# Kernel optimization log

Hardware: AMD Instinct MI355X
Metric: run time of the kernel (lower is better)

The kernel has to match this reference:

```python
import jax, jax.numpy as jnp
import numpy as np

B, C, IMG, PS, S, D, H, HD, L, OUT = 512, 3, 36, 6, 36, 768, 12, 64, 4, 256

def _pos_embedding(seq_len, dim):
    # NOTE: cos at even indices, sin at odd (as in the torch source)
    position = np.arange(seq_len, dtype=np.float32)[:, None]
    div = np.exp(np.arange(0, dim, 2, dtype=np.float32) * -(np.log(10000.0) / dim))
    emb = np.zeros((seq_len, dim), dtype=np.float32)
    emb[:, 0::2] = np.cos(position * div)
    emb[:, 1::2] = np.sin(position * div)
    return jnp.asarray(emb)

def setup_inputs():
    ks = jax.random.split(jax.random.key(0), 10)
    sc = lambda f: 1.0 / np.sqrt(f)
    return {
        'batch': jax.random.normal(ks[0], (B, C, IMG, IMG), jnp.float32),
        'W_patch': jax.random.normal(ks[1], (D, PS * PS), jnp.float32) * sc(PS * PS),
        'b_patch': jnp.zeros((D,), jnp.float32),
        'pos': _pos_embedding(S, D),
        'ln1_g': jnp.ones((L, D), jnp.float32),
        'ln1_b': jnp.zeros((L, D), jnp.float32),
        'Wq': jax.random.normal(ks[2], (L, H, HD, HD), jnp.float32) * sc(HD),
        'bq': jnp.zeros((L, H, HD), jnp.float32),
        'Wk': jax.random.normal(ks[3], (L, H, HD, HD), jnp.float32) * sc(HD),
        'bk': jnp.zeros((L, H, HD), jnp.float32),
        'Wv': jax.random.normal(ks[4], (L, H, HD, HD), jnp.float32) * sc(HD),
        'bv': jnp.zeros((L, H, HD), jnp.float32),
        'ln2_g': jnp.ones((L, D), jnp.float32),
        'ln2_b': jnp.zeros((L, D), jnp.float32),
        'W1': jax.random.normal(ks[5], (L, 2 * D, D), jnp.float32) * sc(D),
        'b1': jnp.zeros((L, 2 * D), jnp.float32),
        'W2': jax.random.normal(ks[6], (L, D, 2 * D), jnp.float32) * sc(2 * D),
        'b2': jnp.zeros((L, D), jnp.float32),
        'W_out': jax.random.normal(ks[7], (OUT, D), jnp.float32) * sc(D),
        'b_out': jnp.zeros((OUT,), jnp.float32),
    }

def _layernorm(x, g, b):
    m = jnp.mean(x, axis=-1, keepdims=True)
    v = jnp.mean((x - m) ** 2, axis=-1, keepdims=True)
    return (x - m) / jnp.sqrt(v + 1e-5) * g + b

def _forward(batch, W_patch, b_patch, pos, ln1_g, ln1_b, Wq, bq, Wk, bk, Wv, bv,
             ln2_g, ln2_b, W1, b1, W2, b2, W_out, b_out):
    b_, c_ = batch.shape[0], batch.shape[1]
    # patchify: (B,C,36,36) -> (B,C,36 patches,36 pixels), matching torch unfold+reshape
    p = batch.reshape(b_, c_, IMG // PS, PS, IMG // PS, PS)
    p = p.transpose(0, 1, 2, 4, 3, 5).reshape(b_, c_, S, PS * PS)
    z = p @ W_patch.T + b_patch + pos  # pos broadcasts over (B,C)
    scale = 1.0 / np.sqrt(HD)
    for l in range(L):
        # pre-LN then batched per-head attention (collapses the python loops)
        h = _layernorm(z, ln1_g[l], ln1_b[l]).reshape(b_, c_, S, H, HD)
        q = jnp.einsum('bcshd,hed->bcshe', h, Wq[l]) + bq[l]
        k = jnp.einsum('bcshd,hed->bcshe', h, Wk[l]) + bk[l]
        v = jnp.einsum('bcshd,hed->bcshe', h, Wv[l]) + bv[l]
        attn = jax.nn.softmax(jnp.einsum('bcshe,bcthe->bchst', q, k) * scale, axis=-1)
        o = jnp.einsum('bchst,bcthe->bcshe', attn, v).reshape(b_, c_, S, D)
        z = z + o
        z = _layernorm(z, ln2_g[l], ln2_b[l])
        z = z + (jax.nn.relu(z @ W1[l].T + b1[l]) @ W2[l].T + b2[l])
    return z @ W_out.T + b_out

def reference(batch, W_patch, b_patch, pos, ln1_g, ln1_b, Wq, bq, Wk, bk, Wv, bv,
              ln2_g, ln2_b, W1, b1, W2, b2, W_out, b_out):
    return _forward(batch, W_patch, b_patch, pos, ln1_g, ln1_b, Wq, bq, Wk, bk, Wv, bv,
                    ln2_g, ln2_b, W1, b1, W2, b2, W_out, b_out)
```

## Files before the change

### kernel.cpp

```cpp
#include <hip/hip_runtime.h>
#include <hip/hip_bf16.h>
#include <cstdint>
#include <cstddef>

typedef __bf16 bf16;
typedef bf16 bf16x8 __attribute__((ext_vector_type(8)));
typedef bf16 bf16x4 __attribute__((ext_vector_type(4)));
typedef float f32x4 __attribute__((ext_vector_type(4)));
typedef unsigned int u32;

#define GLD_LDS16(gptr, lptr)                                                        \
  __builtin_amdgcn_global_load_lds((const __attribute__((address_space(1))) u32*)(gptr), \
                                   (__attribute__((address_space(3))) u32*)(lptr), 16, 0, 0)

static constexpr int S = 36, D = 768, H = 12, HD = 64, DFF = 1536;
static constexpr int BC = 1536;
static constexpr int M = BC * S;
static constexpr int OUTD = 256;

__global__ __launch_bounds__(256) void f2b_kernel(const float* __restrict__ in,
                                                  bf16* __restrict__ out, int n4) {
  int i = blockIdx.x * 256 + threadIdx.x;
  if (i < n4) {
    float4 f = ((const float4*)in)[i];
    bf16x4 o = {(bf16)f.x, (bf16)f.y, (bf16)f.z, (bf16)f.w};
    ((bf16x4*)out)[i] = o;
  }
}

__global__ __launch_bounds__(64) void qk_prep(const float* __restrict__ Wq,
                                              const float* __restrict__ Wk,
                                              const float* __restrict__ bq,
                                              bf16* __restrict__ wb,
                                              float* __restrict__ vkout) {
  int lh = blockIdx.x;
  int e = threadIdx.x;
  __shared__ float Wqs[64][64];
  __shared__ float Wks[64][64];
  const float* wqp = Wq + (size_t)lh * 4096;
  const float* wkp = Wk + (size_t)lh * 4096;
  for (int i = e; i < 4096; i += 64) {
    Wqs[i >> 6][i & 63] = wqp[i];
    Wks[i >> 6][i & 63] = wkp[i];
  }
  __syncthreads();
  float ks[64];
#pragma unroll
  for (int f = 0; f < 64; ++f) ks[f] = Wks[f][e];
  for (int d0 = 0; d0 < 64; d0 += 4) {
    float a0 = 0.f, a1 = 0.f, a2 = 0.f, a3 = 0.f;
#pragma unroll
    for (int f = 0; f < 64; ++f) {
      float4 wq4 = *(const float4*)&Wqs[f][d0];
      a0 += wq4.x * ks[f]; a1 += wq4.y * ks[f];
      a2 += wq4.z * ks[f]; a3 += wq4.w * ks[f];
    }
    bf16x4 o = {(bf16)a0, (bf16)a1, (bf16)a2, (bf16)a3};
    *(bf16x4*)&wb[(size_t)lh * 4096 + e * 64 + d0] = o;
  }
  const float* bqp = bq + lh * 64;
  float acc = 0.f;
#pragma unroll
  for (int f = 0; f < 64; ++f) acc += ks[f] * bqp[f];
  vkout[lh * 64 + e] = acc;
}

__global__ __launch_bounds__(256) void patch_embed(const float* __restrict__ batch,
                                                   const float* __restrict__ Wp,
                                                   const float* __restrict__ bp,
                                                   const float* __restrict__ pos,
                                                   float* __restrict__ z) {
  int bc = blockIdx.x, tid = threadIdx.x;
  __shared__ float p[36][40];
  for (int i = tid; i < 1296; i += 256) {
    float f = batch[(size_t)bc * 1296 + i];
    int row = i / 36, col = i - row * 36;
    p[(row / 6) * 6 + col / 6][(row % 6) * 6 + (col % 6)] = f;
  }
  __syncthreads();
  for (int c0 = 0; c0 < 768; c0 += 256) {
    int d = c0 + tid;
    float wr[36];
    const float4* wp4 = (const float4*)(Wp + (size_t)d * 36);
#pragma unroll
    for (int q = 0; q < 9; ++q) {
      float4 f = wp4[q];
      wr[q * 4] = f.x; wr[q * 4 + 1] = f.y; wr[q * 4 + 2] = f.z; wr[q * 4 + 3] = f.w;
    }
    float gb = bp[d];
    for (int s = 0; s < 36; ++s) {
      float acc = 0.f;
#pragma unroll
      for (int k = 0; k < 36; ++k) acc += p[s][k] * wr[k];
      z[((size_t)bc * 36 + s) * 768 + d] = acc + gb + pos[s * 768 + d];
    }
  }
}

__global__ __launch_bounds__(256) void ln_stats(const float* __restrict__ zin,
                                                float* __restrict__ stats) {
  int row = blockIdx.x * 4 + (threadIdx.x >> 6);
  int lane = threadIdx.x & 63;
  const float* zr = zin + (size_t)row * D;
  float x[12];
#pragma unroll
  for (int i = 0; i < 12; ++i) x[i] = zr[i * 64 + lane];
  float s = 0.f;
#pragma unroll
  for (int i = 0; i < 12; ++i) s += x[i];
#pragma unroll
  for (int off = 32; off >= 1; off >>= 1) s += __shfl_xor(s, off, 64);
  float m = s * (1.f / 768.f);
  float v = 0.f;
#pragma unroll
  for (int i = 0; i < 12; ++i) { float dd = x[i] - m; v += dd * dd; }
#pragma unroll
  for (int off = 32; off >= 1; off >>= 1) v += __shfl_xor(v, off, 64);
  v *= (1.f / 768.f);
  if (lane == 0) {
    stats[(size_t)row * 2] = m;
    stats[(size_t)row * 2 + 1] = rsqrtf(v + 1e-5f);
  }
}

__global__ __launch_bounds__(256) void ln_inplace(float* __restrict__ z,
                                                  const float* __restrict__ g,
                                                  const float* __restrict__ bt) {
  int row = blockIdx.x * 4 + (threadIdx.x >> 6);
  int lane = threadIdx.x & 63;
  float* zr = z + (size_t)row * D;
  float x[12];
#pragma unroll
  for (int i = 0; i < 12; ++i) x[i] = zr[i * 64 + lane];
  float s = 0.f;
#pragma unroll
  for (int i = 0; i < 12; ++i) s += x[i];
#pragma unroll
  for (int off = 32; off >= 1; off >>= 1) s += __shfl_xor(s, off, 64);
  float m = s * (1.f / 768.f);
  float v = 0.f;
#pragma unroll
  for (int i = 0; i < 12; ++i) { float dd = x[i] - m; v += dd * dd; }
#pragma unroll
  for (int off = 32; off >= 1; off >>= 1) v += __shfl_xor(v, off, 64);
  v *= (1.f / 768.f);
  float rstd = rsqrtf(v + 1e-5f);
#pragma unroll
  for (int i = 0; i < 12; ++i) {
    int d = i * 64 + lane;
    zr[d] = (x[i] - m) * rstd * g[d] + bt[d];
  }
}

__global__ __launch_bounds__(64) void attn_kernel(const float* __restrict__ zg,
                                                  const float* __restrict__ stats,
                                                  const float* __restrict__ g1,
                                                  const float* __restrict__ b1_,
                                                  const bf16* __restrict__ Wqk,
                                                  const bf16* __restrict__ Wv,
                                                  const float* __restrict__ vk,
                                                  const float* __restrict__ bv,
                                                  float* __restrict__ z) {
  int head = blockIdx.x;
  int bc = blockIdx.y;
  __shared__ __align__(16) bf16 gb[48 * 72];
  __shared__ __align__(16) bf16 vt[64 * 72];
  int lane = threadIdx.x;
  int lr = lane & 15, quad = lane >> 4;

#pragma unroll
  for (int t0 = 0; t0 < 16; ++t0) vt[lane * 72 + 48 + t0] = (bf16)0.f;

  const float* zsrc = zg + ((size_t)bc * S) * D + head * HD;
  const float* st = stats + (size_t)bc * S * 2;

  float gv[2][8], bvv[2][8];
#pragma unroll
  for (int kt = 0; kt < 2; ++kt) {
    int c0 = head * HD + kt * 32 + quad * 8;
    float4 ga = *(const float4*)(g1 + c0);
    float4 gb2 = *(const float4*)(g1 + c0 + 4);
    float4 ba = *(const float4*)(b1_ + c0);
    float4 bb2 = *(const float4*)(b1_ + c0 + 4);
    gv[kt][0] = ga.x; gv[kt][1] = ga.y; gv[kt][2] = ga.z; gv[kt][3] = ga.w;
    gv[kt][4] = gb2.x; gv[kt][5] = gb2.y; gv[kt][6] = gb2.z; gv[kt][7] = gb2.w;
    bvv[kt][0] = ba.x; bvv[kt][1] = ba.y; bvv[kt][2] = ba.z; bvv[kt][3] = ba.w;
    bvv[kt][4] = bb2.x; bvv[kt][5] = bb2.y; bvv[kt][6] = bb2.z; bvv[kt][7] = bb2.w;
  }

  bf16x8 hfrag[3][2];
#pragma unroll
  for (int mt = 0; mt < 3; ++mt) {
    int srow = mt * 16 + lr;
    if (srow < 36) {
      float mm = st[srow * 2], rr = st[srow * 2 + 1];
#pragma unroll
      for (int kt = 0; kt < 2; ++kt) {
        int c0 = kt * 32 + quad * 8;
        float4 f0 = *(const float4*)(zsrc + (size_t)srow * D + c0);
        float4 f1 = *(const float4*)(zsrc + (size_t)srow * D + c0 + 4);
        float hv[8] = {f0.x, f0.y, f0.z, f0.w, f1.x, f1.y, f1.z, f1.w};
        bf16x8 o;
#pragma unroll
        for (int j = 0; j < 8; ++j) o[j] = (bf16)((hv[j] - mm) * rr * gv[kt][j] + bvv[kt][j]);
        hfrag[mt][kt] = o;
      }
    } else {
#pragma unroll
      for (int kt = 0; kt < 2; ++kt) {
        bf16x8 o;
#pragma unroll
        for (int j = 0; j < 8; ++j) o[j] = (bf16)0.f;
        hfrag[mt][kt] = o;
      }
    }
  }

  float vkv[2][8];
#pragma unroll
  for (int kt = 0; kt < 2; ++kt) {
    int c0 = head * 64 + kt * 32 + quad * 8;
    float4 va = *(const float4*)(vk + c0);
    float4 vb2 = *(const float4*)(vk + c0 + 4);
    vkv[kt][0] = va.x; vkv[kt][1] = va.y; vkv[kt][2] = va.z; vkv[kt][3] = va.w;
    vkv[kt][4] = vb2.x; vkv[kt][5] = vb2.y; vkv[kt][6] = vb2.z; vkv[kt][7] = vb2.w;
  }
  float tv[3];
#pragma unroll
  for (int mt = 0; mt < 3; ++mt) {
    float sp = 0.f;
#pragma unroll
    for (int kt = 0; kt < 2; ++kt)
#pragma unroll
      for (int j = 0; j < 8; ++j) sp += (float)hfrag[mt][kt][j] * vkv[kt][j];
    sp += __shfl_xor(sp, 16, 64);
    sp += __shfl_xor(sp, 32, 64);
    tv[mt] = sp;
  }

  const bf16* Wm[2] = {Wqk + (size_t)head * 4096, Wv + (size_t)head * 4096};
  const float* bvp = bv + head * 64;
  for (int p = 0; p < 2; ++p) {
    bf16x8 bfr[4][2];
#pragma unroll
    for (int nt = 0; nt < 4; ++nt)
#pragma unroll
      for (int kt = 0; kt < 2; ++kt)
        bfr[nt][kt] = *(const bf16x8*)(Wm[p] + (nt * 16 + lr) * 64 + kt * 32 + quad * 8);
#pragma unroll
    for (int mt = 0; mt < 3; ++mt) {
      f32x4 acc[4] = {};
#pragma unroll
      for (int kt = 0; kt < 2; ++kt)
#pragma unroll
        for (int nt = 0; nt < 4; ++nt)
          acc[nt] = __builtin_amdgcn_mfma_f32_16x16x32_bf16(hfrag[mt][kt], bfr[nt][kt], acc[nt], 0, 0, 0);
#pragma unroll
      for (int nt = 0; nt < 4; ++nt) {
        float bb = (p == 1) ? bvp[nt * 16 + lr] : 0.f;
#pragma unroll
        for (int r = 0; r < 4; ++r) {
          int s2 = mt * 16 + quad * 4 + r;
          int e = nt * 16 + lr;
          float val = acc[nt][r] + bb;
          if (p == 0) gb[s2 * 72 + e] = (bf16)val;
          else vt[e * 72 + s2] = (bf16)val;
        }
      }
    }
  }
  __syncthreads();

  f32x4 sc[3][3];
#pragma unroll
  for (int mt = 0; mt < 3; ++mt)
#pragma unroll
    for (int nt = 0; nt < 3; ++nt) {
      f32x4 a = {};
#pragma unroll
      for (int kt = 0; kt < 2; ++kt) {
        bf16x8 af = *(const bf16x8*)&gb[(mt * 16 + lr) * 72 + kt * 32 + quad * 8];
        a = __builtin_amdgcn_mfma_f32_16x16x32_bf16(af, hfrag[nt][kt], a, 0, 0, 0);
      }
      int t = nt * 16 + lr;
#pragma unroll
      for (int r = 0; r < 4; ++r) {
        float v = (a[r] + tv[nt]) * 0.125f;
        if (t >= 36) v = -1e30f;
        sc[mt][nt][r] = v;
      }
    }
  __syncthreads();

#pragma unroll
  for (int mt = 0; mt < 3; ++mt) {
    float mx[4], sum[4];
#pragma unroll
    for (int r = 0; r < 4; ++r)
      mx[r] = fmaxf(fmaxf(sc[mt][0][r], sc[mt][1][r]), sc[mt][2][r]);
#pragma unroll
    for (int r = 0; r < 4; ++r)
#pragma unroll
      for (int off = 8; off >= 1; off >>= 1) mx[r] = fmaxf(mx[r], __shfl_xor(mx[r], off, 64));
#pragma unroll
    for (int r = 0; r < 4; ++r) sum[r] = 0.f;
#pragma unroll
    for (int nt = 0; nt < 3; ++nt)
#pragma unroll
      for (int r = 0; r < 4; ++r) {
        float e = __expf(sc[mt][nt][r] - mx[r]);
        sc[mt][nt][r] = e;
        sum[r] += e;
      }
#pragma unroll
    for (int r = 0; r < 4; ++r)
#pragma unroll
      for (int off = 8; off >= 1; off >>= 1) sum[r] += __shfl_xor(sum[r], off, 64);
#pragma unroll
    for (int nt = 0; nt < 4; ++nt)
#pragma unroll
      for (int r = 0; r < 4; ++r) {
        int s2 = mt * 16 + quad * 4 + r;
        int t = nt * 16 + lr;
        float pv = (nt < 3) ? sc[mt][nt][r] / sum[r] : 0.f;
        gb[s2 * 72 + t] = (bf16)pv;
      }
  }
  __syncthreads();

#pragma unroll
  for (int mt = 0; mt < 3; ++mt) {
    f32x4 o[4] = {};
#pragma unroll
    for (int kt = 0; kt < 2; ++kt) {
      bf16x8 a = *(const bf16x8*)&gb[(mt * 16 + lr) * 72 + kt * 32 + quad * 8];
#pragma unroll
      for (int nt = 0; nt < 4; ++nt) {
        bf16x8 b = *(const bf16x8*)&vt[(nt * 16 + lr) * 72 + kt * 32 + quad * 8];
        o[nt] = __builtin_amdgcn_mfma_f32_16x16x32_bf16(a, b, o[nt], 0, 0, 0);
      }
    }
#pragma unroll
    for (int nt = 0; nt < 4; ++nt)
#pragma unroll
      for (int r = 0; r < 4; ++r) {
        int s2 = mt * 16 + quad * 4 + r;
        if (s2 < 36) {
          int e = nt * 16 + lr;
          size_t idx = ((size_t)bc * S + s2) * D + head * HD + e;
          z[idx] += o[nt][r];
        }
      }
  }
}

template <int N, int K, int MODE, int AF32>
__global__ __launch_bounds__(256) void gemm_bt(const void* __restrict__ A,
                                               const bf16* __restrict__ Bw,
                                               const float* __restrict__ bias,
                                               const float* __restrict__ res,
                                               void* __restrict__ outp) {
  constexpr int BK = 64;
  __shared__ __align__(16) bf16 As[128 * BK];
  __shared__ __align__(16) bf16 Bs[128 * BK];
  int tid = threadIdx.x;
  int bn = blockIdx.x, bm = blockIdx.y;
  const bf16* Abf = (const bf16*)A + (size_t)bm * 128 * K;
  const float* Af = (const float*)A + (size_t)bm * 128 * K;
  const bf16* Bb = Bw + (size_t)bn * 128 * K;
  int lane = tid & 63, wave = tid >> 6;
  int wm = (wave >> 1) * 64, wn = (wave & 1) * 64;
  int lr = lane & 15, quad = lane >> 4;
  f32x4 acc[4][4] = {};
  for (int k0 = 0; k0 < K; k0 += BK) {
    if (AF32) {
#pragma unroll
      for (int r = 0; r < 8; ++r) {
        int c = r * 256 + tid;
        int row = c >> 4, col4 = (c & 15) * 4;
        float4 f = *(const float4*)(Af + (size_t)row * K + k0 + col4);
        bf16x4 o = {(bf16)f.x, (bf16)f.y, (bf16)f.z, (bf16)f.w};
        *(bf16x4*)&As[row * BK + col4] = o;
      }
    } else {
#pragma unroll
      for (int r = 0; r < 4; ++r) {
        int c = r * 256 + tid;
        int row = c >> 3, col = (c & 7) * 8;
        GLD_LDS16(Abf + (size_t)row * K + k0 + col, &As[c * 8]);
      }
    }
#pragma unroll
    for (int r = 0; r < 4; ++r) {
      int c = r * 256 + tid;
      int row = c >> 3, col = (c & 7) * 8;
      GLD_LDS16(Bb + (size_t)row * K + k0 + col, &Bs[c * 8]);
    }
    __syncthreads();
#pragma unroll
    for (int kt = 0; kt < 2; ++kt) {
      bf16x8 af[4], bfr[4];
#pragma unroll
      for (int mt = 0; mt < 4; ++mt) af[mt] = *(const bf16x8*)&As[(wm + mt * 16 + lr) * BK + kt * 32 + quad * 8];
#pragma unroll
      for (int nt = 0; nt < 4; ++nt) bfr[nt] = *(const bf16x8*)&Bs[(wn + nt * 16 + lr) * BK + kt * 32 + quad * 8];
#pragma unroll
      for (int mt = 0; mt < 4; ++mt)
#pragma unroll
        for (int nt = 0; nt < 4; ++nt)
          acc[mt][nt] = __builtin_amdgcn_mfma_f32_16x16x32_bf16(af[mt], bfr[nt], acc[mt][nt], 0, 0, 0);
    }
    __syncthreads();
  }
  int row0 = bm * 128 + wm + quad * 4;
  int col0 = bn * 128 + wn + lr;
#pragma unroll
  for (int mt = 0; mt < 4; ++mt)
#pragma unroll
    for (int nt = 0; nt < 4; ++nt) {
      int col = col0 + nt * 16;
      float bv = bias[col];
#pragma unroll
      for (int r = 0; r < 4; ++r) {
        size_t idx = (size_t)(row0 + mt * 16 + r) * N + col;
        float v = acc[mt][nt][r] + bv;
        if (MODE == 0) ((bf16*)outp)[idx] = (bf16)fmaxf(v, 0.f);
        else if (MODE == 1) ((float*)outp)[idx] = v + res[idx];
        else ((float*)outp)[idx] = v;
      }
    }
}

extern "C" void kernel_launch(void* const* d_in, const int* in_sizes, int n_in,
                              void* d_out, int out_size, void* d_ws, size_t ws_size,
                              hipStream_t stream) {
  const float* batch   = (const float*)d_in[0];
  const float* W_patch = (const float*)d_in[1];
  const float* b_patch = (const float*)d_in[2];
  const float* pos     = (const float*)d_in[3];
  const float* ln1_g   = (const float*)d_in[4];
  const float* ln1_b   = (const float*)d_in[5];
  const float* Wq      = (const float*)d_in[6];
  const float* bq      = (const float*)d_in[7];
  const float* Wk      = (const float*)d_in[8];
  const float* bk      = (const float*)d_in[9];
  const float* Wv      = (const float*)d_in[10];
  const float* bv      = (const float*)d_in[11];
  const float* ln2_g   = (const float*)d_in[12];
  const float* ln2_b   = (const float*)d_in[13];
  const float* W1      = (const float*)d_in[14];
  const float* b1      = (const float*)d_in[15];
  const float* W2      = (const float*)d_in[16];
  const float* b2      = (const float*)d_in[17];
  const float* W_out   = (const float*)d_in[18];
  const float* b_out   = (const float*)d_in[19];
  float* out = (float*)d_out;
  (void)bk;

  char* ws = (char*)d_ws;
  size_t off = 0;
  float* z     = (float*)(ws + off); off += (size_t)M * D * 4;
  float* stats = (float*)(ws + off); off += (size_t)M * 2 * 4;
  bf16* wqk_b = (bf16*)(ws + off);   off += (size_t)4 * H * 4096 * 2;
  bf16* wv_b = (bf16*)(ws + off);    off += (size_t)4 * H * 4096 * 2;
  float* vk_f = (float*)(ws + off);  off += (size_t)4 * H * 64 * 4;
  bf16* w1_b = (bf16*)(ws + off);    off += (size_t)4 * DFF * D * 2;
  bf16* w2_b = (bf16*)(ws + off);    off += (size_t)4 * D * DFF * 2;
  bf16* wo_b = (bf16*)(ws + off);    off += (size_t)OUTD * D * 2;
  bf16* act  = (bf16*)(ws + off);

  size_t avail = ws_size > off ? ws_size - off : (size_t)0;
  long long rcl = (long long)(avail / ((size_t)DFF * 2));
  int rc = (rcl > (long long)M) ? M : (int)rcl;
  rc = (rc / 128) * 128;
  if (rc <= 0) rc = 128;

  qk_prep<<<48, 64, 0, stream>>>(Wq, Wk, bq, wqk_b, vk_f);
  f2b_kernel<<<192, 256, 0, stream>>>(Wv, wv_b, 49152);
  f2b_kernel<<<4608, 256, 0, stream>>>(W1, w1_b, 1179648);
  f2b_kernel<<<4608, 256, 0, stream>>>(W2, w2_b, 1179648);
  f2b_kernel<<<192, 256, 0, stream>>>(W_out, wo_b, 49152);

  patch_embed<<<BC, 256, 0, stream>>>(batch, W_patch, b_patch, pos, z);

  for (int l = 0; l < 4; ++l) {
    ln_stats<<<M / 4, 256, 0, stream>>>(z, stats);
    attn_kernel<<<dim3(H, BC), 64, 0, stream>>>(z, stats, ln1_g + l * D, ln1_b + l * D,
        wqk_b + (size_t)l * H * 4096, wv_b + (size_t)l * H * 4096,
        vk_f + (size_t)l * H * 64, bv + (size_t)l * H * 64, z);
    ln_inplace<<<M / 4, 256, 0, stream>>>(z, ln2_g + l * D, ln2_b + l * D);
    for (int m0 = 0; m0 < M; m0 += rc) {
      int mr = (M - m0 < rc) ? (M - m0) : rc;
      gemm_bt<DFF, D, 0, 1><<<dim3(DFF / 128, mr / 128), 256, 0, stream>>>(
          z + (size_t)m0 * D, w1_b + (size_t)l * DFF * D, b1 + l * DFF, nullptr, act);
      gemm_bt<D, DFF, 1, 0><<<dim3(D / 128, mr / 128), 256, 0, stream>>>(
          act, w2_b + (size_t)l * D * DFF, b2 + l * D, z + (size_t)m0 * D, z + (size_t)m0 * D);
    }
  }

  gemm_bt<OUTD, D, 2, 1><<<dim3(OUTD / 128, M / 128), 256, 0, stream>>>(
      z, wo_b, b_out, nullptr, out);
}
```

Measured before the change: 3.440 ms.

## Fuse layernorm stats into FFN down-proj epilogue and remap GEMM block order

```diff
diff --git a/kernel.cpp b/kernel.cpp
--- a/kernel.cpp
+++ b/kernel.cpp
@@ -25,6 +25,22 @@
     float4 f = ((const float4*)in)[i];
     bf16x4 o = {(bf16)f.x, (bf16)f.y, (bf16)f.z, (bf16)f.w};
     ((bf16x4*)out)[i] = o;
+  }
+}
+
+__global__ __launch_bounds__(256) void zerok(float* __restrict__ p, int n) {
+  int i = blockIdx.x * 256 + threadIdx.x;
+  if (i < n) p[i] = 0.f;
+}
+__global__ __launch_bounds__(256) void stats_fin(const float* __restrict__ sacc,
+                                                 float* __restrict__ stats, int n) {
+  int i = blockIdx.x * 256 + threadIdx.x;
+  if (i < n) {
+    float sm = sacc[(size_t)i * 2] * (1.f / 768.f);
+    float sq = sacc[(size_t)i * 2 + 1] * (1.f / 768.f);
+    float var = sq - sm * sm;
+    stats[(size_t)i * 2] = sm;
+    stats[(size_t)i * 2 + 1] = rsqrtf(var + 1e-5f);
   }
 }
 
@@ -359,12 +375,21 @@
                                                const bf16* __restrict__ Bw,
                                                const float* __restrict__ bias,
                                                const float* __restrict__ res,
-                                               void* __restrict__ outp) {
+                                               void* __restrict__ outp,
+                                               float* __restrict__ sacc) {
   constexpr int BK = 64;
   __shared__ __align__(16) bf16 As[128 * BK];
   __shared__ __align__(16) bf16 Bs[128 * BK];
   int tid = threadIdx.x;
   int bn = blockIdx.x, bm = blockIdx.y;
+  if ((gridDim.y & 7) == 0) {
+    int gx = gridDim.x, gy = gridDim.y;
+    int h = bm * gx + bn;
+    int x = h & 7, k = h >> 3;
+    int gpc = gy >> 3;
+    bm = x * gpc + k / gx;
+    bn = k - (k / gx) * gx;
+  }
   const bf16* Abf = (const bf16*)A + (size_t)bm * 128 * K;
   const float* Af = (const float*)A + (size_t)bm * 128 * K;
   const bf16* Bb = Bw + (size_t)bn * 128 * K;
@@ -414,21 +439,48 @@
   }
   int row0 = bm * 128 + wm + quad * 4;
   int col0 = bn * 128 + wn + lr;
-#pragma unroll
-  for (int mt = 0; mt < 4; ++mt)
-#pragma unroll
-    for (int nt = 0; nt < 4; ++nt) {
-      int col = col0 + nt * 16;
-      float bv = bias[col];
+  if (MODE == 4) {
+#pragma unroll
+    for (int mt = 0; mt < 4; ++mt)
 #pragma unroll
       for (int r = 0; r < 4; ++r) {
-        size_t idx = (size_t)(row0 + mt * 16 + r) * N + col;
-        float v = acc[mt][nt][r] + bv;
-        if (MODE == 0) ((bf16*)outp)[idx] = (bf16)fmaxf(v, 0.f);
-        else if (MODE == 1) ((float*)outp)[idx] = v + res[idx];
-        else ((float*)outp)[idx] = v;
-      }
-    }
+        int row = row0 + mt * 16 + r;
+        float rs = 0.f, rq = 0.f;
+#pragma unroll
+        for (int nt = 0; nt < 4; ++nt) {
+          int col = col0 + nt * 16;
+          size_t idx = (size_t)row * N + col;
+          float o = acc[mt][nt][r] + bias[col] + res[idx];
+          ((float*)outp)[idx] = o;
+          rs += o; rq += o * o;
+        }
+#pragma unroll
+        for (int off = 8; off >= 1; off >>= 1) {
+          rs += __shfl_xor(rs, off, 64);
+          rq += __shfl_xor(rq, off, 64);
+        }
+        if (lr == 0) {
+          atomicAdd(&sacc[(size_t)row * 2], rs);
+          atomicAdd(&sacc[(size_t)row * 2 + 1], rq);
+        }
+      }
+  } else {
+#pragma unroll
+    for (int mt = 0; mt < 4; ++mt)
+#pragma unroll
+      for (int nt = 0; nt < 4; ++nt) {
+        int col = col0 + nt * 16;
+        float bv = bias[col];
+#pragma unroll
+        for (int r = 0; r < 4; ++r) {
+          size_t idx = (size_t)(row0 + mt * 16 + r) * N + col;
+          float v = acc[mt][nt][r] + bv;
+          if (MODE == 0) ((bf16*)outp)[idx] = (bf16)fmaxf(v, 0.f);
+          else if (MODE == 1) ((float*)outp)[idx] = v + res[idx];
+          else ((float*)outp)[idx] = v;
+        }
+      }
+  }
 }
 
 extern "C" void kernel_launch(void* const* d_in, const int* in_sizes, int n_in,
@@ -461,6 +513,7 @@
   size_t off = 0;
   float* z     = (float*)(ws + off); off += (size_t)M * D * 4;
   float* stats = (float*)(ws + off); off += (size_t)M * 2 * 4;
+  float* sacc  = (float*)(ws + off); off += (size_t)M * 2 * 4;
   bf16* wqk_b = (bf16*)(ws + off);   off += (size_t)4 * H * 4096 * 2;
   bf16* wv_b = (bf16*)(ws + off);    off += (size_t)4 * H * 4096 * 2;
   float* vk_f = (float*)(ws + off);  off += (size_t)4 * H * 64 * 4;
@@ -472,7 +525,7 @@
   size_t avail = ws_size > off ? ws_size - off : (size_t)0;
   long long rcl = (long long)(avail / ((size_t)DFF * 2));
   int rc = (rcl > (long long)M) ? M : (int)rcl;
-  rc = (rc / 128) * 128;
+  rc = (rc / 1024) * 1024;
   if (rc <= 0) rc = 128;
 
   qk_prep<<<48, 64, 0, stream>>>(Wq, Wk, bq, wqk_b, vk_f);
@@ -482,22 +535,30 @@
   f2b_kernel<<<192, 256, 0, stream>>>(W_out, wo_b, 49152);
 
   patch_embed<<<BC, 256, 0, stream>>>(batch, W_patch, b_patch, pos, z);
+  ln_stats<<<M / 4, 256, 0, stream>>>(z, stats);
 
   for (int l = 0; l < 4; ++l) {
-    ln_stats<<<M / 4, 256, 0, stream>>>(z, stats);
     attn_kernel<<<dim3(H, BC), 64, 0, stream>>>(z, stats, ln1_g + l * D, ln1_b + l * D,
         wqk_b + (size_t)l * H * 4096, wv_b + (size_t)l * H * 4096,
         vk_f + (size_t)l * H * 64, bv + (size_t)l * H * 64, z);
     ln_inplace<<<M / 4, 256, 0, stream>>>(z, ln2_g + l * D, ln2_b + l * D);
+    if (l < 3) zerok<<<(M * 2 + 255) / 256, 256, 0, stream>>>(sacc, M * 2);
     for (int m0 = 0; m0 < M; m0 += rc) {
       int mr = (M - m0 < rc) ? (M - m0) : rc;
       gemm_bt<DFF, D, 0, 1><<<dim3(DFF / 128, mr / 128), 256, 0, stream>>>(
-          z + (size_t)m0 * D, w1_b + (size_t)l * DFF * D, b1 + l * DFF, nullptr, act);
-      gemm_bt<D, DFF, 1, 0><<<dim3(D / 128, mr / 128), 256, 0, stream>>>(
-          act, w2_b + (size_t)l * D * DFF, b2 + l * D, z + (size_t)m0 * D, z + (size_t)m0 * D);
-    }
+          z + (size_t)m0 * D, w1_b + (size_t)l * DFF * D, b1 + l * DFF, nullptr, act, nullptr);
+      if (l < 3)
+        gemm_bt<D, DFF, 4, 0><<<dim3(D / 128, mr / 128), 256, 0, stream>>>(
+            act, w2_b + (size_t)l * D * DFF, b2 + l * D, z + (size_t)m0 * D,
+            z + (size_t)m0 * D, sacc + (size_t)m0 * 2);
+      else
+        gemm_bt<D, DFF, 1, 0><<<dim3(D / 128, mr / 128), 256, 0, stream>>>(
+            act, w2_b + (size_t)l * D * DFF, b2 + l * D, z + (size_t)m0 * D,
+            z + (size_t)m0 * D, nullptr);
+    }
+    if (l < 3) stats_fin<<<(M + 255) / 256, 256, 0, stream>>>(sacc, stats, M);
   }
 
   gemm_bt<OUTD, D, 2, 1><<<dim3(OUTD / 128, M / 128), 256, 0, stream>>>(
-      z, wo_b, b_out, nullptr, out);
-}
+      z, wo_b, b_out, nullptr, out, nullptr);
+}
```

New measurement: 3.395 ms. Within noise of the previous version (-1.3%).
